# Optimization experiments

Measured on AMD Instinct MI355X. Metric: run time of the kernel, lower is better.

The kernel has to match this reference:

```python
import jax, jax.numpy as jnp
import numpy as np

IN_DIM = 4096
OUT_DIM = 4096
CODEBOOK_SIZE = 65536
LAYER_ID = 3
HASH_A, HASH_B, HASH_C = 10007, 20011, 40009
SIGN_HASH_A, SIGN_HASH_B, SIGN_HASH_C = 4099, 6151, 14887
SIGNED_HASH = True
BATCH = 8192


def _hash_tables():
    i = jnp.arange(OUT_DIM, dtype=jnp.int64 if jax.config.jax_enable_x64 else jnp.int32)[:, None]
    j = jnp.arange(IN_DIM, dtype=i.dtype)[None, :]
    idx = (i * HASH_A + j * HASH_B + LAYER_ID * HASH_C) % CODEBOOK_SIZE
    bits = (i * SIGN_HASH_A + j * SIGN_HASH_B + LAYER_ID * SIGN_HASH_C) % 2
    signs = bits.astype(jnp.float32) * 2.0 - 1.0
    return idx, signs


def setup_inputs() -> dict:
    key = jax.random.key(0)
    kx, kc = jax.random.split(key)
    x = jax.random.normal(kx, (BATCH, IN_DIM), dtype=jnp.float32)
    codebook = jax.random.normal(kc, (CODEBOOK_SIZE,), dtype=jnp.float32) * 0.01
    bias = jnp.zeros((OUT_DIM,), dtype=jnp.float32)
    return {"x": x, "codebook": codebook, "bias": bias}


def reference(x, codebook, bias):
    idx, signs = _hash_tables()  # [out_dim, in_dim] each
    weight = codebook[idx]  # gather from tiny codebook -> [out_dim, in_dim]
    if SIGNED_HASH:
        weight = weight * signs.astype(weight.dtype)
    # F.linear: y = x @ W^T + b
    return jnp.einsum('bi,oi->bo', x, weight) + bias
```

## Files before the change

kernel.cpp:

```cpp
#include <hip/hip_runtime.h>
#include <hip/hip_bf16.h>

constexpr int M_ = 8192;
constexpr int N_ = 4096;
constexpr int K_ = 4096;
constexpr int CBOOK = 65536;
constexpr int HA = 10007, HB = 20011;
constexpr int HC3 = 3 * 40009;

constexpr int C0 = 197;

constexpr int BM = 256, BN = 256, BK = 32;
constexpr int NKT = K_ / BK;

using bf16x8 = __bf16 __attribute__((ext_vector_type(8)));
using f32x4  = float __attribute__((ext_vector_type(4)));
using u16x8  = unsigned short __attribute__((ext_vector_type(8)));

typedef __attribute__((address_space(3))) void lds_void_t;
typedef const __attribute__((address_space(1))) void gbl_void_t;

static __device__ __forceinline__ unsigned short f2bf(float f) {
    __bf16 h = (__bf16)f;
    return __builtin_bit_cast(unsigned short, h);
}

constexpr int P2N   = 8 * 65536;
constexpr int P2B   = P2N / 256;

__global__ __launch_bounds__(256) void prep_p2(const float* __restrict__ cb,
                                               unsigned short* __restrict__ P2p) {
    const int t = blockIdx.x * 256 + threadIdx.x;
    const int p = t >> 16;
    const int i = t & 65535;
    const int u = i + p;
    float v = cb[(u * HB + HC3) & (CBOOK - 1)];
    if (u & 1) v = -v;
    P2p[t] = f2bf(v);
}

constexpr int GENB  = N_ * K_ / 8 / 256;
constexpr int CONVB = M_ * K_ / 8 / 256;

__global__ __launch_bounds__(256) void prep_main(const float* __restrict__ x,
                                                 const unsigned short* __restrict__ P2p,
                                                 unsigned short* __restrict__ Wf,
                                                 unsigned short* __restrict__ xb) {
    const int b = blockIdx.x;
    if (b < GENB) {
        const int t    = b * 256 + threadIdx.x;
        const int slot = t & 1023;
        const int kt   = (t >> 10) & 127;
        const int nb   = t >> 17;
        const int row  = slot >> 2;
        const int key  = (row >> 1) & 3;
        const int n  = (nb << 8) + row;
        const int k0 = (kt << 5) + (((slot & 3) ^ key) << 3);
        const int u0 = (C0 * n + k0) & (CBOOK - 1);
        const u16x8 w = *reinterpret_cast<const u16x8*>(
            P2p + ((u0 & 7) << 16) + (u0 & 65528));
        *reinterpret_cast<u16x8*>(&Wf[(size_t)t * 8]) = w;
    } else {
        const size_t t = (size_t)(b - GENB) * 256 + threadIdx.x;
        const float4* p = reinterpret_cast<const float4*>(x) + t * 2;
        const float4 a = p[0], c = p[1];
        u16x8 out;
        out[0] = f2bf(a.x); out[1] = f2bf(a.y); out[2] = f2bf(a.z); out[3] = f2bf(a.w);
        out[4] = f2bf(c.x); out[5] = f2bf(c.y); out[6] = f2bf(c.z); out[7] = f2bf(c.w);
        reinterpret_cast<u16x8*>(xb)[t] = out;
    }
}

__global__ __launch_bounds__(512, 2) void gemm_kernel(
        const unsigned short* __restrict__ A,
        const unsigned short* __restrict__ Wf,
        const float* __restrict__ bias,
        float* __restrict__ C) {
    __shared__ __align__(16) unsigned short sm[4 * 8192 * 2];
    unsigned short* As = sm;
    unsigned short* Bs = sm + 4 * 8192;

    const int tid  = threadIdx.x;
    const int lane = tid & 63;
    const int w    = tid >> 6;
    const int wm   = w >> 2;
    const int wn   = w & 3;
    const int m0 = blockIdx.y * BM;
    const int n0 = blockIdx.x * BN;

    const int quad = lane >> 4;
    const int l16  = lane & 15;

    const int sblk = (lane & 3) ^ ((lane >> 3) & 3);
    const unsigned short* aLane =
        A + (size_t)(m0 + w * 16 + (lane >> 2)) * K_ + sblk * 8;
    const unsigned short* bLane =
        Wf + (size_t)blockIdx.x * NKT * 8192 + tid * 8;

    const int rblk = (quad ^ ((l16 >> 1) & 3)) * 8;
    const unsigned short* aRd = As + (wm * 128 + l16) * 32 + rblk;
    const unsigned short* bRd = Bs + (wn * 64 + l16) * 32 + rblk;

    f32x4 acc[8][4] = {};
    bf16x8 bfr[4], afr[8];

    auto STAGE = [&](int kt, int bs) {
#pragma unroll
        for (int r = 0; r < 2; ++r) {
            __builtin_amdgcn_global_load_lds(
                (gbl_void_t*)(aLane + (size_t)r * 128 * K_ + (size_t)kt * BK),
                (lds_void_t*)(As + bs * 8192 + (r * 512 + w * 64) * 8), 16, 0, 0);
            __builtin_amdgcn_global_load_lds(
                (gbl_void_t*)(bLane + (size_t)kt * 8192 + r * 4096),
                (lds_void_t*)(Bs + bs * 8192 + (r * 512 + w * 64) * 8), 16, 0, 0);
        }
    };

    STAGE(0, 0); STAGE(1, 1); STAGE(2, 2);
    asm volatile("s_waitcnt vmcnt(8)" ::: "memory");
    __builtin_amdgcn_s_barrier();
#pragma unroll
    for (int nt = 0; nt < 4; ++nt)
        bfr[nt] = *reinterpret_cast<const bf16x8*>(bRd + nt * 512);
#pragma unroll
    for (int mt = 0; mt < 8; ++mt)
        afr[mt] = *reinterpret_cast<const bf16x8*>(aRd + mt * 512);

    for (int kt0 = 0; kt0 < NKT; kt0 += 4) {
#pragma unroll
        for (int s = 0; s < 4; ++s) {
            const int kt = kt0 + s;
            if (kt + 2 < NKT)      asm volatile("s_waitcnt vmcnt(4)" ::: "memory");
            else if (kt + 1 < NKT) asm volatile("s_waitcnt vmcnt(0)" ::: "memory");
            __builtin_amdgcn_s_barrier();

            if (kt + 3 < NKT) STAGE(kt + 3, (s + 3) & 3);

            const int rs = ((s + 1) & 3) * 8192;
            __builtin_amdgcn_s_setprio(1);
#pragma unroll
            for (int mt = 0; mt < 8; ++mt) {
#pragma unroll
                for (int nt = 0; nt < 4; ++nt)
                    acc[mt][nt] = __builtin_amdgcn_mfma_f32_16x16x32_bf16(
                        afr[mt], bfr[nt], acc[mt][nt], 0, 0, 0);
                afr[mt] = *reinterpret_cast<const bf16x8*>(aRd + rs + mt * 512);
            }
            __builtin_amdgcn_s_setprio(0);
#pragma unroll
            for (int nt = 0; nt < 4; ++nt)
                bfr[nt] = *reinterpret_cast<const bf16x8*>(bRd + rs + nt * 512);
        }
    }

#pragma unroll
    for (int nt = 0; nt < 4; ++nt) {
        const int col = n0 + wn * 64 + nt * 16 + l16;
        const float bv = bias[col];
#pragma unroll
        for (int mt = 0; mt < 8; ++mt) {
            const int rowb = m0 + wm * 128 + mt * 16 + quad * 4;
#pragma unroll
            for (int r = 0; r < 4; ++r)
                C[(size_t)(rowb + r) * N_ + col] = acc[mt][nt][r] + bv;
        }
    }
}

__global__ __launch_bounds__(256) void naive_kernel(const float* __restrict__ x,
                                                    const float* __restrict__ cb,
                                                    const float* __restrict__ bias,
                                                    float* __restrict__ out) {
    const size_t t = (size_t)blockIdx.x * 256 + threadIdx.x;
    const int row = (int)(t / N_);
    const int col = (int)(t % N_);
    float s = bias[col];
    const float* xr = x + (size_t)row * K_;
    const int h = col * HA + HC3;
    for (int i = 0; i < K_; ++i) {
        float v = cb[(h + i * HB) & (CBOOK - 1)];
        s += xr[i] * (((col ^ i) & 1) ? -v : v);
    }
    out[t] = s;
}

extern "C" void kernel_launch(void* const* d_in, const int* in_sizes, int n_in,
                              void* d_out, int out_size, void* d_ws, size_t ws_size,
                              hipStream_t stream) {
    const float* x    = (const float*)d_in[0];
    const float* cb   = (const float*)d_in[1];
    const float* bias = (const float*)d_in[2];
    float* out = (float*)d_out;

    const size_t wBytes = (size_t)N_ * K_ * sizeof(unsigned short);
    const size_t xBytes = (size_t)M_ * K_ * sizeof(unsigned short);
    const size_t pBytes = (size_t)P2N * sizeof(unsigned short);

    if (ws_size >= wBytes + xBytes + pBytes) {
        unsigned short* Wf  = (unsigned short*)d_ws;
        unsigned short* xb  = (unsigned short*)((char*)d_ws + wBytes);
        unsigned short* P2p = (unsigned short*)((char*)d_ws + wBytes + xBytes);
        prep_p2<<<P2B, 256, 0, stream>>>(cb, P2p);
        prep_main<<<GENB + CONVB, 256, 0, stream>>>(x, P2p, Wf, xb);
        gemm_kernel<<<dim3(N_ / BN, M_ / BM), 512, 0, stream>>>(xb, Wf, bias, out);
    } else {
        naive_kernel<<<(int)((size_t)M_ * N_ / 256), 256, 0, stream>>>(x, cb, bias, out);
    }
}
```

Before: 447.7 us.

## Load weight fragments directly from global into registers, bypassing LDS

The prep kernel now writes the generated weight matrix in MFMA fragment order, 16 rows by 32 k per 64-lane tile. This lets each wave load its B operands straight from global memory into double-buffered registers. The B tile no longer goes through LDS, which halves shared memory use and removes the B LDS reads. In exchange, the two waves sharing an N slice each fetch the same B data, which raises global/L2 traffic. The wait counting is also reworked to a fixed vmcnt(6), which looks fragile in the final iterations where fewer loads are issued.

```diff
diff --git a/kernel.cpp b/kernel.cpp
--- a/kernel.cpp
+++ b/kernel.cpp
@@ -48,14 +48,12 @@
                                                  unsigned short* __restrict__ xb) {
     const int b = blockIdx.x;
     if (b < GENB) {
-        const int t    = b * 256 + threadIdx.x;
-        const int slot = t & 1023;
-        const int kt   = (t >> 10) & 127;
-        const int nb   = t >> 17;
-        const int row  = slot >> 2;
-        const int key  = (row >> 1) & 3;
-        const int n  = (nb << 8) + row;
-        const int k0 = (kt << 5) + (((slot & 3) ^ key) << 3);
+        const int t     = b * 256 + threadIdx.x;
+        const int lane  = t & 63;
+        const int kt    = (t >> 6) & 127;
+        const int ntile = t >> 13;
+        const int n  = (ntile << 4) + (lane & 15);
+        const int k0 = (kt << 5) + ((lane >> 4) << 3);
         const int u0 = (C0 * n + k0) & (CBOOK - 1);
         const u16x8 w = *reinterpret_cast<const u16x8*>(
             P2p + ((u0 & 7) << 16) + (u0 & 65528));
@@ -76,9 +74,7 @@
         const unsigned short* __restrict__ Wf,
         const float* __restrict__ bias,
         float* __restrict__ C) {
-    __shared__ __align__(16) unsigned short sm[4 * 8192 * 2];
-    unsigned short* As = sm;
-    unsigned short* Bs = sm + 4 * 8192;
+    __shared__ __align__(16) unsigned short As[4 * 8192];
 
     const int tid  = threadIdx.x;
     const int lane = tid & 63;
@@ -94,34 +90,34 @@
     const int sblk = (lane & 3) ^ ((lane >> 3) & 3);
     const unsigned short* aLane =
         A + (size_t)(m0 + w * 16 + (lane >> 2)) * K_ + sblk * 8;
-    const unsigned short* bLane =
-        Wf + (size_t)blockIdx.x * NKT * 8192 + tid * 8;
+    const unsigned short* bWave =
+        Wf + (size_t)(blockIdx.x * 16 + wn * 4) * NKT * 512 + lane * 8;
 
     const int rblk = (quad ^ ((l16 >> 1) & 3)) * 8;
     const unsigned short* aRd = As + (wm * 128 + l16) * 32 + rblk;
-    const unsigned short* bRd = Bs + (wn * 64 + l16) * 32 + rblk;
 
     f32x4 acc[8][4] = {};
-    bf16x8 bfr[4], afr[8];
+    bf16x8 afr[8];
+    bf16x8 bfrE[4], bfrO[4];
 
     auto STAGE = [&](int kt, int bs) {
 #pragma unroll
-        for (int r = 0; r < 2; ++r) {
+        for (int r = 0; r < 2; ++r)
             __builtin_amdgcn_global_load_lds(
                 (gbl_void_t*)(aLane + (size_t)r * 128 * K_ + (size_t)kt * BK),
                 (lds_void_t*)(As + bs * 8192 + (r * 512 + w * 64) * 8), 16, 0, 0);
-            __builtin_amdgcn_global_load_lds(
-                (gbl_void_t*)(bLane + (size_t)kt * 8192 + r * 4096),
-                (lds_void_t*)(Bs + bs * 8192 + (r * 512 + w * 64) * 8), 16, 0, 0);
-        }
     };
+    auto BLOAD = [&](int kt, bf16x8 (&dst)[4]) {
+#pragma unroll
+        for (int nt = 0; nt < 4; ++nt)
+            dst[nt] = *reinterpret_cast<const bf16x8*>(
+                bWave + ((size_t)nt * NKT + kt) * 512);
+    };
 
     STAGE(0, 0); STAGE(1, 1); STAGE(2, 2);
-    asm volatile("s_waitcnt vmcnt(8)" ::: "memory");
+    BLOAD(0, bfrE);
+    asm volatile("s_waitcnt vmcnt(0)" ::: "memory");
     __builtin_amdgcn_s_barrier();
-#pragma unroll
-    for (int nt = 0; nt < 4; ++nt)
-        bfr[nt] = *reinterpret_cast<const bf16x8*>(bRd + nt * 512);
 #pragma unroll
     for (int mt = 0; mt < 8; ++mt)
         afr[mt] = *reinterpret_cast<const bf16x8*>(aRd + mt * 512);
@@ -130,11 +126,13 @@
 #pragma unroll
         for (int s = 0; s < 4; ++s) {
             const int kt = kt0 + s;
-            if (kt + 2 < NKT)      asm volatile("s_waitcnt vmcnt(4)" ::: "memory");
-            else if (kt + 1 < NKT) asm volatile("s_waitcnt vmcnt(0)" ::: "memory");
+            asm volatile("s_waitcnt vmcnt(6)" ::: "memory");
             __builtin_amdgcn_s_barrier();
 
             if (kt + 3 < NKT) STAGE(kt + 3, (s + 3) & 3);
+            if (kt + 1 < NKT) {
+                if (s & 1) BLOAD(kt + 1, bfrE); else BLOAD(kt + 1, bfrO);
+            }
 
             const int rs = ((s + 1) & 3) * 8192;
             __builtin_amdgcn_s_setprio(1);
@@ -143,13 +141,11 @@
 #pragma unroll
                 for (int nt = 0; nt < 4; ++nt)
                     acc[mt][nt] = __builtin_amdgcn_mfma_f32_16x16x32_bf16(
-                        afr[mt], bfr[nt], acc[mt][nt], 0, 0, 0);
+                        afr[mt], (s & 1) ? bfrO[nt] : bfrE[nt],
+                        acc[mt][nt], 0, 0, 0);
                 afr[mt] = *reinterpret_cast<const bf16x8*>(aRd + rs + mt * 512);
             }
             __builtin_amdgcn_s_setprio(0);
-#pragma unroll
-            for (int nt = 0; nt < 4; ++nt)
-                bfr[nt] = *reinterpret_cast<const bf16x8*>(bRd + rs + nt * 512);
         }
     }
 
```

Result: slower. 480.0 us (+7.2%).

## Double-buffer B fragments in registers and halve barrier frequency in GEMM loop

Applied to the files above, without the earlier changes.

The B-operand register fragments are split into even and odd sets, so next-step B loads from LDS are issued inside the MFMA loop instead of after it. The main loop now waits and barriers only every second k-step and issues two tile stages at a time. The intent is to hide LDS read latency behind MFMAs and cut barrier overhead. In exchange, each wait drains all outstanding global loads (vmcnt(0)), which shortens the effective prefetch lead and adds fragment registers.

```diff
diff --git a/kernel.cpp b/kernel.cpp
--- a/kernel.cpp
+++ b/kernel.cpp
@@ -102,7 +102,8 @@
     const unsigned short* bRd = Bs + (wn * 64 + l16) * 32 + rblk;
 
     f32x4 acc[8][4] = {};
-    bf16x8 bfr[4], afr[8];
+    bf16x8 afr[8];
+    bf16x8 bfrE[4], bfrO[4];
 
     auto STAGE = [&](int kt, int bs) {
 #pragma unroll
@@ -117,11 +118,11 @@
     };
 
     STAGE(0, 0); STAGE(1, 1); STAGE(2, 2);
-    asm volatile("s_waitcnt vmcnt(8)" ::: "memory");
+    asm volatile("s_waitcnt vmcnt(0)" ::: "memory");
     __builtin_amdgcn_s_barrier();
 #pragma unroll
     for (int nt = 0; nt < 4; ++nt)
-        bfr[nt] = *reinterpret_cast<const bf16x8*>(bRd + nt * 512);
+        bfrE[nt] = *reinterpret_cast<const bf16x8*>(bRd + nt * 512);
 #pragma unroll
     for (int mt = 0; mt < 8; ++mt)
         afr[mt] = *reinterpret_cast<const bf16x8*>(aRd + mt * 512);
@@ -129,12 +130,17 @@
     for (int kt0 = 0; kt0 < NKT; kt0 += 4) {
 #pragma unroll
         for (int s = 0; s < 4; ++s) {
-            const int kt = kt0 + s;
-            if (kt + 2 < NKT)      asm volatile("s_waitcnt vmcnt(4)" ::: "memory");
-            else if (kt + 1 < NKT) asm volatile("s_waitcnt vmcnt(0)" ::: "memory");
-            __builtin_amdgcn_s_barrier();
-
-            if (kt + 3 < NKT) STAGE(kt + 3, (s + 3) & 3);
+            if ((s & 1) == 0) {
+                asm volatile("s_waitcnt vmcnt(0)" ::: "memory");
+                __builtin_amdgcn_s_barrier();
+                if (s == 0) {
+                    if (kt0 + 3 < NKT) STAGE(kt0 + 3, 3);
+                    if (kt0 + 4 < NKT) STAGE(kt0 + 4, 0);
+                } else {
+                    if (kt0 + 5 < NKT) STAGE(kt0 + 5, 1);
+                    if (kt0 + 6 < NKT) STAGE(kt0 + 6, 2);
+                }
+            }
 
             const int rs = ((s + 1) & 3) * 8192;
             __builtin_amdgcn_s_setprio(1);
@@ -143,13 +149,19 @@
 #pragma unroll
                 for (int nt = 0; nt < 4; ++nt)
                     acc[mt][nt] = __builtin_amdgcn_mfma_f32_16x16x32_bf16(
-                        afr[mt], bfr[nt], acc[mt][nt], 0, 0, 0);
+                        afr[mt], (s & 1) ? bfrO[nt] : bfrE[nt],
+                        acc[mt][nt], 0, 0, 0);
                 afr[mt] = *reinterpret_cast<const bf16x8*>(aRd + rs + mt * 512);
+                if ((mt & 1) == 0) {
+                    if (s & 1)
+                        bfrE[mt >> 1] = *reinterpret_cast<const bf16x8*>(
+                            bRd + rs + (mt >> 1) * 512);
+                    else
+                        bfrO[mt >> 1] = *reinterpret_cast<const bf16x8*>(
+                            bRd + rs + (mt >> 1) * 512);
+                }
             }
             __builtin_amdgcn_s_setprio(0);
-#pragma unroll
-            for (int nt = 0; nt < 4; ++nt)
-                bfr[nt] = *reinterpret_cast<const bf16x8*>(bRd + rs + nt * 512);
         }
     }
 
```

Measured after the change: 453.4 us. Within noise of the previous version (+1.3%).

## Switch GEMM to 32x32x16 MFMA with fragment-ordered prepacked A and B tiles

Applied to the files above, without the earlier changes.

Replaces the 16x16x32 bf16 MFMA tiling with 32x32x16 instructions, so each wave issues 16 larger MFMAs per k-tile instead of 32 small ones. The prep kernel now writes both the bf16 x and the hashed weights in a fragment-ordered tiled layout, so LDS reads are simple lane-contiguous loads with no XOR swizzle. The goal is fewer MFMA and LDS instructions and better matrix-core throughput. The cost is a strided gather in the x conversion, and the prologue now waits with vmcnt(0), which drains all three prefetched stages.

```diff
diff --git a/kernel.cpp b/kernel.cpp
--- a/kernel.cpp
+++ b/kernel.cpp
@@ -14,7 +14,7 @@
 constexpr int NKT = K_ / BK;
 
 using bf16x8 = __bf16 __attribute__((ext_vector_type(8)));
-using f32x4  = float __attribute__((ext_vector_type(4)));
+using f32x16 = float __attribute__((ext_vector_type(16)));
 using u16x8  = unsigned short __attribute__((ext_vector_type(8)));
 
 typedef __attribute__((address_space(3))) void lds_void_t;
@@ -51,23 +51,35 @@
         const int t    = b * 256 + threadIdx.x;
         const int slot = t & 1023;
         const int kt   = (t >> 10) & 127;
-        const int nb   = t >> 17;
-        const int row  = slot >> 2;
-        const int key  = (row >> 1) & 3;
-        const int n  = (nb << 8) + row;
-        const int k0 = (kt << 5) + (((slot & 3) ^ key) << 3);
+        const int strip = t >> 17;
+        const int l  = slot & 63;
+        const int s  = (slot >> 6) & 1;
+        const int nt = (slot >> 7) & 1;
+        const int q  = (slot >> 8) & 3;
+        const int n  = (strip << 8) + (q << 6) + (nt << 5) + (l & 31);
+        const int k0 = (kt << 5) + (s << 4) + ((l >> 5) << 3);
         const int u0 = (C0 * n + k0) & (CBOOK - 1);
         const u16x8 w = *reinterpret_cast<const u16x8*>(
             P2p + ((u0 & 7) << 16) + (u0 & 65528));
         *reinterpret_cast<u16x8*>(&Wf[(size_t)t * 8]) = w;
     } else {
-        const size_t t = (size_t)(b - GENB) * 256 + threadIdx.x;
-        const float4* p = reinterpret_cast<const float4*>(x) + t * 2;
+        const int t    = (b - GENB) * 256 + threadIdx.x;
+        const int slot = t & 1023;
+        const int kt   = (t >> 10) & 127;
+        const int band = t >> 17;
+        const int l  = slot & 63;
+        const int s  = (slot >> 6) & 1;
+        const int mt = (slot >> 7) & 3;
+        const int h  = (slot >> 9) & 1;
+        const int row = (band << 8) + (h << 7) + (mt << 5) + (l & 31);
+        const int k   = (kt << 5) + (s << 4) + ((l >> 5) << 3);
+        const float4* p = reinterpret_cast<const float4*>(
+            x + (size_t)row * K_ + k);
         const float4 a = p[0], c = p[1];
         u16x8 out;
         out[0] = f2bf(a.x); out[1] = f2bf(a.y); out[2] = f2bf(a.z); out[3] = f2bf(a.w);
         out[4] = f2bf(c.x); out[5] = f2bf(c.y); out[6] = f2bf(c.z); out[7] = f2bf(c.w);
-        reinterpret_cast<u16x8*>(xb)[t] = out;
+        *reinterpret_cast<u16x8*>(&xb[(size_t)t * 8]) = out;
     }
 }
 
@@ -87,82 +99,97 @@
     const int wn   = w & 3;
     const int m0 = blockIdx.y * BM;
     const int n0 = blockIdx.x * BN;
-
-    const int quad = lane >> 4;
-    const int l16  = lane & 15;
-
-    const int sblk = (lane & 3) ^ ((lane >> 3) & 3);
-    const unsigned short* aLane =
-        A + (size_t)(m0 + w * 16 + (lane >> 2)) * K_ + sblk * 8;
-    const unsigned short* bLane =
-        Wf + (size_t)blockIdx.x * NKT * 8192 + tid * 8;
-
-    const int rblk = (quad ^ ((l16 >> 1) & 3)) * 8;
-    const unsigned short* aRd = As + (wm * 128 + l16) * 32 + rblk;
-    const unsigned short* bRd = Bs + (wn * 64 + l16) * 32 + rblk;
-
-    f32x4 acc[8][4] = {};
-    bf16x8 bfr[4], afr[8];
+    const int l31 = lane & 31;
+    const int lhi = lane >> 5;
+
+    const unsigned short* xbBand =
+        A + (size_t)blockIdx.y * (NKT * 8192) + tid * 8;
+    const unsigned short* wfStrip =
+        Wf + (size_t)blockIdx.x * (NKT * 8192) + tid * 8;
+    const unsigned short* aRd = As + wm * 4096 + lane * 8;
+    const unsigned short* bRd = Bs + wn * 2048 + lane * 8;
+
+    f32x16 acc[4][2] = {};
+    bf16x8 afr[2][4], bfr[2][2];
 
     auto STAGE = [&](int kt, int bs) {
 #pragma unroll
         for (int r = 0; r < 2; ++r) {
             __builtin_amdgcn_global_load_lds(
-                (gbl_void_t*)(aLane + (size_t)r * 128 * K_ + (size_t)kt * BK),
+                (gbl_void_t*)(xbBand + (size_t)kt * 8192 + r * 4096),
                 (lds_void_t*)(As + bs * 8192 + (r * 512 + w * 64) * 8), 16, 0, 0);
             __builtin_amdgcn_global_load_lds(
-                (gbl_void_t*)(bLane + (size_t)kt * 8192 + r * 4096),
+                (gbl_void_t*)(wfStrip + (size_t)kt * 8192 + r * 4096),
                 (lds_void_t*)(Bs + bs * 8192 + (r * 512 + w * 64) * 8), 16, 0, 0);
         }
     };
 
     STAGE(0, 0); STAGE(1, 1); STAGE(2, 2);
-    asm volatile("s_waitcnt vmcnt(8)" ::: "memory");
+    asm volatile("s_waitcnt vmcnt(0)" ::: "memory");
     __builtin_amdgcn_s_barrier();
 #pragma unroll
-    for (int nt = 0; nt < 4; ++nt)
-        bfr[nt] = *reinterpret_cast<const bf16x8*>(bRd + nt * 512);
-#pragma unroll
-    for (int mt = 0; mt < 8; ++mt)
-        afr[mt] = *reinterpret_cast<const bf16x8*>(aRd + mt * 512);
+    for (int s = 0; s < 2; ++s) {
+#pragma unroll
+        for (int mt = 0; mt < 4; ++mt)
+            afr[s][mt] = *reinterpret_cast<const bf16x8*>(aRd + (mt * 2 + s) * 512);
+#pragma unroll
+        for (int nt = 0; nt < 2; ++nt)
+            bfr[s][nt] = *reinterpret_cast<const bf16x8*>(bRd + (nt * 2 + s) * 512);
+    }
 
     for (int kt0 = 0; kt0 < NKT; kt0 += 4) {
 #pragma unroll
-        for (int s = 0; s < 4; ++s) {
-            const int kt = kt0 + s;
+        for (int s4 = 0; s4 < 4; ++s4) {
+            const int kt = kt0 + s4;
             if (kt + 2 < NKT)      asm volatile("s_waitcnt vmcnt(4)" ::: "memory");
             else if (kt + 1 < NKT) asm volatile("s_waitcnt vmcnt(0)" ::: "memory");
             __builtin_amdgcn_s_barrier();
 
-            if (kt + 3 < NKT) STAGE(kt + 3, (s + 3) & 3);
-
-            const int rs = ((s + 1) & 3) * 8192;
+            if (kt + 3 < NKT) STAGE(kt + 3, (s4 + 3) & 3);
+
+            const int rs = ((s4 + 1) & 3) * 8192;
             __builtin_amdgcn_s_setprio(1);
 #pragma unroll
-            for (int mt = 0; mt < 8; ++mt) {
-#pragma unroll
-                for (int nt = 0; nt < 4; ++nt)
-                    acc[mt][nt] = __builtin_amdgcn_mfma_f32_16x16x32_bf16(
-                        afr[mt], bfr[nt], acc[mt][nt], 0, 0, 0);
-                afr[mt] = *reinterpret_cast<const bf16x8*>(aRd + rs + mt * 512);
+            for (int mt = 0; mt < 4; ++mt) {
+                acc[mt][0] = __builtin_amdgcn_mfma_f32_32x32x16_bf16(
+                    afr[0][mt], bfr[0][0], acc[mt][0], 0, 0, 0);
+                acc[mt][1] = __builtin_amdgcn_mfma_f32_32x32x16_bf16(
+                    afr[0][mt], bfr[0][1], acc[mt][1], 0, 0, 0);
+                afr[0][mt] = *reinterpret_cast<const bf16x8*>(
+                    aRd + rs + (mt * 2 + 0) * 512);
             }
+#pragma unroll
+            for (int nt = 0; nt < 2; ++nt)
+                bfr[0][nt] = *reinterpret_cast<const bf16x8*>(
+                    bRd + rs + (nt * 2 + 0) * 512);
+#pragma unroll
+            for (int mt = 0; mt < 4; ++mt) {
+                acc[mt][0] = __builtin_amdgcn_mfma_f32_32x32x16_bf16(
+                    afr[1][mt], bfr[1][0], acc[mt][0], 0, 0, 0);
+                acc[mt][1] = __builtin_amdgcn_mfma_f32_32x32x16_bf16(
+                    afr[1][mt], bfr[1][1], acc[mt][1], 0, 0, 0);
+                afr[1][mt] = *reinterpret_cast<const bf16x8*>(
+                    aRd + rs + (mt * 2 + 1) * 512);
+            }
+#pragma unroll
+            for (int nt = 0; nt < 2; ++nt)
+                bfr[1][nt] = *reinterpret_cast<const bf16x8*>(
+                    bRd + rs + (nt * 2 + 1) * 512);
             __builtin_amdgcn_s_setprio(0);
-#pragma unroll
-            for (int nt = 0; nt < 4; ++nt)
-                bfr[nt] = *reinterpret_cast<const bf16x8*>(bRd + rs + nt * 512);
         }
     }
 
 #pragma unroll
-    for (int nt = 0; nt < 4; ++nt) {
-        const int col = n0 + wn * 64 + nt * 16 + l16;
+    for (int nt = 0; nt < 2; ++nt) {
+        const int col = n0 + wn * 64 + nt * 32 + l31;
         const float bv = bias[col];
 #pragma unroll
-        for (int mt = 0; mt < 8; ++mt) {
-            const int rowb = m0 + wm * 128 + mt * 16 + quad * 4;
-#pragma unroll
-            for (int r = 0; r < 4; ++r)
-                C[(size_t)(rowb + r) * N_ + col] = acc[mt][nt][r] + bv;
+        for (int mt = 0; mt < 4; ++mt) {
+            const int rowb = m0 + wm * 128 + mt * 32 + lhi * 4;
+#pragma unroll
+            for (int rg = 0; rg < 16; ++rg)
+                C[(size_t)(rowb + (rg & 3) + 8 * (rg >> 2)) * N_ + col] =
+                    acc[mt][nt][rg] + bv;
         }
     }
 }
```

Result: slower. 472.3 us (+5.5%).
